# Performance work log

Measured on AMD Instinct MI355X. Metric: run time of the kernel, lower is better.

## Reference

```python
import jax, jax.numpy as jnp
import numpy as np

N_EMBD = 2048
HEAD_DIM = 128
N_CTX = 2048
BATCH = 8
SEQ = 2048


def setup_inputs() -> dict:
    key = jax.random.key(0)
    ks = jax.random.split(key, 7)
    s = 1.0 / np.sqrt(N_EMBD)
    x = jax.random.normal(ks[0], (BATCH, SEQ, N_EMBD), dtype=jnp.float32)
    # torch Linear params: weight (out, in), bias (out,)
    Wq = jax.random.uniform(ks[1], (HEAD_DIM, N_EMBD), jnp.float32, -s, s)
    bq = jax.random.uniform(ks[2], (HEAD_DIM,), jnp.float32, -s, s)
    Wk = jax.random.uniform(ks[3], (HEAD_DIM, N_EMBD), jnp.float32, -s, s)
    bk = jax.random.uniform(ks[4], (HEAD_DIM,), jnp.float32, -s, s)
    Wv = jax.random.uniform(ks[5], (HEAD_DIM, N_EMBD), jnp.float32, -s, s)
    bv = jax.random.uniform(ks[6], (HEAD_DIM,), jnp.float32, -s, s)
    return {"x": x, "Wq": Wq, "bq": bq, "Wk": Wk, "bk": bk, "Wv": Wv, "bv": bv}


def reference(x, Wq, bq, Wk, bk, Wv, bv):
    # projections: y = x @ W^T + b
    q = jnp.einsum('bse,de->bsd', x, Wq) + bq  # (B, S, D)
    k = jnp.einsum('bse,de->bsd', x, Wk) + bk
    v = jnp.einsum('bse,de->bsd', x, Wv) + bv
    seq = x.shape[1]
    scores = jnp.einsum('bqd,bkd->bqk', q, k)  # (B, S, S)
    # causal mask: strictly-upper-triangular positions set to -inf (before scaling, as in source)
    causal = jnp.triu(jnp.ones((seq, seq), dtype=bool), k=1)
    scores = jnp.where(causal[None, :, :], -jnp.inf, scores)
    # NOTE: source scales by sqrt(seq_size), not sqrt(head_dim)
    weight = jax.nn.softmax(scores / jnp.sqrt(jnp.float32(seq)), axis=-1)
    return jnp.einsum('bqk,bkd->bqd', weight, v)
```

## Files before the change

kernel.cpp:

```cpp
#include <hip/hip_runtime.h>
#include <cmath>

#define BATCH 8
#define SEQ   2048
#define NEMB  2048
#define HD    128
#define NROWS (BATCH * SEQ)

typedef __bf16 v8bf __attribute__((ext_vector_type(8)));
typedef float  f32x4 __attribute__((ext_vector_type(4)));

union U8 { v8bf v; __bf16 b[8]; unsigned short e[8]; };

__device__ inline void async16(void* lds, const void* g) {
  __builtin_amdgcn_global_load_lds(
      (const __attribute__((address_space(1))) unsigned int*)g,
      (__attribute__((address_space(3))) unsigned int*)lds, 16, 0, 0);
}

__device__ inline v8bf cvt8(float4 a, float4 b) {
  U8 u;
  u.b[0] = (__bf16)a.x; u.b[1] = (__bf16)a.y; u.b[2] = (__bf16)a.z; u.b[3] = (__bf16)a.w;
  u.b[4] = (__bf16)b.x; u.b[5] = (__bf16)b.y; u.b[6] = (__bf16)b.z; u.b[7] = (__bf16)b.w;
  return u.v;
}

__global__ __launch_bounds__(256) void wconv_kernel(
    const float* __restrict__ Wq, const float* __restrict__ Wk,
    const float* __restrict__ Wv, __bf16* __restrict__ out) {
  const int id = blockIdx.x;
  const int proj = id >> 6, blk = id & 63;
  const float* __restrict__ W = proj == 0 ? Wq : proj == 1 ? Wk : Wv;
  __bf16* __restrict__ o = out + (size_t)proj * (HD * NEMB);
  const int base = blk * 4096 + threadIdx.x * 16;
  const float4* s = (const float4*)(W + base);
  float4 f0 = s[0], f1 = s[1], f2 = s[2], f3 = s[3];
  *(v8bf*)(o + base) = cvt8(f0, f1);
  *(v8bf*)(o + base + 8) = cvt8(f2, f3);
}

__global__ __launch_bounds__(256, 3) void qkv_proj_kernel(
    const float* __restrict__ x, const __bf16* __restrict__ Wb,
    const float* __restrict__ bq, const float* __restrict__ bk,
    const float* __restrict__ bv,
    __bf16* __restrict__ Qb, __bf16* __restrict__ Kb, __bf16* __restrict__ Vb)
{
  const int bid0 = blockIdx.x;
  const int bid = ((bid0 & 7) * 96) + (bid0 >> 3);
  const int mt = bid / 3;
  const int proj = bid % 3;
  const __bf16* __restrict__ W = Wb + (size_t)proj * (HD * NEMB);
  const float* __restrict__ bias = proj == 0 ? bq : proj == 1 ? bk : bv;
  __bf16* __restrict__ Out = proj == 0 ? Qb : proj == 1 ? Kb : Vb;
  const int m0 = mt * 64;

  __shared__ __bf16 Asm[64 * 64];
  __shared__ __bf16 Bsm[128 * 64];

  const int t = threadIdx.x, lane = t & 63, w = t >> 6;
  const int wm = w >> 1, wn = w & 1;
  const int hi = lane >> 4, lo = lane & 15;

  const int arow = t >> 2, aq = t & 3;
  const float* axp = x + (size_t)(m0 + arow) * NEMB + aq * 16;
  char* aw0 = (char*)Asm + arow * 128 + (((aq * 2)     ^ (arow & 7)) << 4);
  char* aw1 = (char*)Asm + arow * 128 + (((aq * 2 + 1) ^ (arow & 7)) << 4);

  const __bf16* pb[4];
#pragma unroll
  for (int i = 0; i < 4; ++i) {
    const int r = (w * 4 + i) * 8 + (lane >> 3);
    const int c = (lane & 7) ^ (r & 7);
    pb[i] = W + (size_t)r * NEMB + c * 8;
  }

  f32x4 acc[2][4];
  const f32x4 fz = {0.f, 0.f, 0.f, 0.f};
#pragma unroll
  for (int m = 0; m < 2; ++m)
#pragma unroll
    for (int n = 0; n < 4; ++n) acc[m][n] = fz;

  float4 fa0, fa1, fa2, fa3;
  auto ALOAD = [&](int tt) {
    const float* p = axp + tt * 64;
    fa0 = *(const float4*)(p);
    fa1 = *(const float4*)(p + 4);
    fa2 = *(const float4*)(p + 8);
    fa3 = *(const float4*)(p + 12);
  };

  const int NT = NEMB / 64;
  ALOAD(0);
  for (int tt = 0; tt < NT; ++tt) {
    __syncthreads();
    {
      const int k0 = tt * 64;
#pragma unroll
      for (int i = 0; i < 4; ++i) async16((char*)Bsm + (w * 4 + i) * 1024, pb[i] + k0);
      *(v8bf*)aw0 = cvt8(fa0, fa1);
      *(v8bf*)aw1 = cvt8(fa2, fa3);
    }
    __syncthreads();
    if (tt + 1 < NT) ALOAD(tt + 1);

#pragma unroll
    for (int kk = 0; kk < 2; ++kk) {
      v8bf a[2], b[4];
      const int kc = kk * 4 + hi;
#pragma unroll
      for (int m = 0; m < 2; ++m) {
        const int r = wm * 32 + m * 16 + lo;
        a[m] = *(const v8bf*)((const char*)Asm + r * 128 + ((kc ^ (r & 7)) << 4));
      }
#pragma unroll
      for (int n = 0; n < 4; ++n) {
        const int r = wn * 64 + n * 16 + lo;
        b[n] = *(const v8bf*)((const char*)Bsm + r * 128 + ((kc ^ (r & 7)) << 4));
      }
#pragma unroll
      for (int m = 0; m < 2; ++m)
#pragma unroll
        for (int n = 0; n < 4; ++n)
          acc[m][n] = __builtin_amdgcn_mfma_f32_16x16x32_bf16(a[m], b[n], acc[m][n], 0, 0, 0);
    }
  }

#pragma unroll
  for (int n = 0; n < 4; ++n) {
    const int col = wn * 64 + n * 16 + lo;
    const float bi = bias[col];
#pragma unroll
    for (int m = 0; m < 2; ++m) {
#pragma unroll
      for (int r = 0; r < 4; ++r) {
        const int row = m0 + wm * 32 + m * 16 + hi * 4 + r;
        Out[(size_t)row * HD + col] = (__bf16)(acc[m][n][r] + bi);
      }
    }
  }
}

__global__ __launch_bounds__(256) void attn_kernel(
    const __bf16* __restrict__ Qb, const __bf16* __restrict__ Kb,
    const __bf16* __restrict__ Vb, float* __restrict__ Opart,
    float* __restrict__ Ml)
{
  const int bid0 = blockIdx.x;
  const int bid = ((bid0 & 7) << 6) + (bid0 >> 3);
  const int b = bid >> 6;
  const int qs = bid & 63;
  const int qt = qs >> 1;
  const int s  = qs & 1;
  const int q0 = qt * 64;
  const int half = (qt + 2) >> 1;
  const int kv_beg = s ? half : 0;
  const int kv_end = s ? (qt + 1) : half;
  const int nst = kv_end - kv_beg;

  const int t = threadIdx.x, lane = t & 63, w = t >> 6;
  const int hi = lane >> 4, lo = lane & 15;

  __shared__ __bf16 Ksm[2][64 * 128];
  __shared__ __bf16 Vtsm[2][128 * 64];
  __shared__ __bf16 Psm[4][16 * 64];

  v8bf aQ[4];
  {
    const __bf16* qp = Qb + ((size_t)(b * SEQ + q0 + w * 16 + lo)) * HD + hi * 8;
#pragma unroll
    for (int kk = 0; kk < 4; ++kk) aQ[kk] = *(const v8bf*)(qp + kk * 32);
  }

  const __bf16* kga[4];
#pragma unroll
  for (int i = 0; i < 4; ++i) {
    const int r = (w * 4 + i) * 4 + (lane >> 4);
    const int c = (lane & 15) ^ (r & 7);
    kga[i] = Kb + ((size_t)(b * SEQ) + r) * HD + c * 8;
  }

  const int keyg = t >> 4, dg = t & 15;
  U8 vv[4];

  f32x4 accO[8];
  const f32x4 fz = {0.f, 0.f, 0.f, 0.f};
#pragma unroll
  for (int n = 0; n < 8; ++n) accO[n] = fz;
  float m_s[4], l_s[4];
#pragma unroll
  for (int r = 0; r < 4; ++r) { m_s[r] = -INFINITY; l_s[r] = 0.f; }

  const float scale = 0.022097086912079608f;

  if (nst > 0) {
    auto STAGE_K = [&](int kv, int buf) {
      const size_t off = (size_t)kv * 64 * HD;
      char* kb = (char*)&Ksm[buf][0];
#pragma unroll
      for (int i = 0; i < 4; ++i) async16(kb + (w * 4 + i) * 1024, kga[i] + off);
    };
    auto LOAD_V = [&](int kv) {
      const __bf16* vp = Vb + ((size_t)(b * SEQ + kv * 64 + keyg * 4)) * HD + dg * 8;
#pragma unroll
      for (int j = 0; j < 4; ++j) vv[j].v = *(const v8bf*)(vp + (size_t)j * HD);
    };
    auto WRITE_VT = [&](int buf) {
      char* vb2 = (char*)&Vtsm[buf][0];
#pragma unroll
      for (int dd = 0; dd < 8; ++dd) {
        const int d = (dd + dg) & 7;
        ushort4 pk = make_ushort4(vv[0].e[d], vv[1].e[d], vv[2].e[d], vv[3].e[d]);
        const int row = dg * 8 + d;
        *(ushort4*)(vb2 + row * 128 + ((keyg * 8) ^ ((row & 7) << 4))) = pk;
      }
    };

    STAGE_K(kv_beg, 0);
    LOAD_V(kv_beg);
    WRITE_VT(0);
    __syncthreads();

    for (int t2 = 0; t2 < nst; ++t2) {
      const int kv = kv_beg + t2;
      const int cur = t2 & 1;
      const bool more = (t2 + 1 < nst);
      if (more) { STAGE_K(kv + 1, cur ^ 1); LOAD_V(kv + 1); }

      f32x4 accS[4];
#pragma unroll
      for (int n = 0; n < 4; ++n) accS[n] = fz;
      const char* ksm = (const char*)&Ksm[cur][0];
#pragma unroll
      for (int kk = 0; kk < 4; ++kk) {
        const int cb = kk * 64 + hi * 16;
        v8bf bk[4];
#pragma unroll
        for (int n = 0; n < 4; ++n) {
          const int r = n * 16 + lo;
          bk[n] = *(const v8bf*)(ksm + r * 256 + (cb ^ ((r & 7) << 4)));
        }
#pragma unroll
        for (int n = 0; n < 4; ++n)
          accS[n] = __builtin_amdgcn_mfma_f32_16x16x32_bf16(aQ[kk], bk[n], accS[n], 0, 0, 0);
      }

      float sv[4][4];
      const bool diag = (kv == qt);
#pragma unroll
      for (int n = 0; n < 4; ++n)
#pragma unroll
        for (int r = 0; r < 4; ++r) {
          float v = accS[n][r] * scale;
          if (diag) {
            const int key = kv * 64 + n * 16 + lo;
            const int qr = q0 + w * 16 + hi * 4 + r;
            if (key > qr) v = -INFINITY;
          }
          sv[n][r] = v;
        }

      float mx[4];
#pragma unroll
      for (int r = 0; r < 4; ++r) {
        mx[r] = fmaxf(fmaxf(sv[0][r], sv[1][r]), fmaxf(sv[2][r], sv[3][r]));
#pragma unroll
        for (int off = 1; off < 16; off <<= 1)
          mx[r] = fmaxf(mx[r], __shfl_xor(mx[r], off));
      }
      float corr[4], p[4][4], rs[4];
#pragma unroll
      for (int r = 0; r < 4; ++r) {
        const float mnew = fmaxf(m_s[r], mx[r]);
        corr[r] = __expf(m_s[r] - mnew);
        m_s[r] = mnew;
        rs[r] = 0.f;
      }
#pragma unroll
      for (int n = 0; n < 4; ++n)
#pragma unroll
        for (int r = 0; r < 4; ++r) {
          p[n][r] = __expf(sv[n][r] - m_s[r]);
          rs[r] += p[n][r];
        }
#pragma unroll
      for (int r = 0; r < 4; ++r) {
#pragma unroll
        for (int off = 1; off < 16; off <<= 1) rs[r] += __shfl_xor(rs[r], off);
        l_s[r] = l_s[r] * corr[r] + rs[r];
      }
#pragma unroll
      for (int n = 0; n < 8; ++n)
#pragma unroll
        for (int r = 0; r < 4; ++r) accO[n][r] *= corr[r];

#pragma unroll
      for (int n = 0; n < 4; ++n)
#pragma unroll
        for (int r = 0; r < 4; ++r) {
          const int row = hi * 4 + r;
          __bf16 h = (__bf16)p[n][r];
          *(unsigned short*)((char*)&Psm[w][0] + row * 128 +
                             (((n * 16 + lo) * 2) ^ ((row & 7) << 4))) =
              __builtin_bit_cast(unsigned short, h);
        }

      if (more) WRITE_VT(cur ^ 1);

      const char* vsm = (const char*)&Vtsm[cur][0];
#pragma unroll
      for (int k2 = 0; k2 < 2; ++k2) {
        const int cb = k2 * 64 + hi * 16;
        const v8bf aP = *(const v8bf*)((const char*)&Psm[w][0] + lo * 128 + (cb ^ ((lo & 7) << 4)));
#pragma unroll
        for (int n = 0; n < 8; ++n) {
          const int r = n * 16 + lo;
          const v8bf bv = *(const v8bf*)(vsm + r * 128 + (cb ^ ((r & 7) << 4)));
          accO[n] = __builtin_amdgcn_mfma_f32_16x16x32_bf16(aP, bv, accO[n], 0, 0, 0);
        }
      }
      if (more) __syncthreads();
    }
  }

#pragma unroll
  for (int r = 0; r < 4; ++r) {
    const int qr = q0 + w * 16 + hi * 4 + r;
    float* op = Opart + ((size_t)s * NROWS + b * SEQ + qr) * HD + lo;
#pragma unroll
    for (int n = 0; n < 8; ++n) op[n * 16] = accO[n][r];
    if (lo == 0) {
      float* mlp = Ml + ((size_t)s * NROWS + b * SEQ + qr) * 2;
      mlp[0] = m_s[r];
      mlp[1] = l_s[r];
    }
  }
}

__global__ __launch_bounds__(256) void combine_kernel(
    const float* __restrict__ Opart, const float* __restrict__ Ml,
    float* __restrict__ out)
{
  const int idx = blockIdx.x * 256 + threadIdx.x;
  const int row = idx >> 1, h = idx & 1;
  const float m0 = Ml[(size_t)row * 2],           l0 = Ml[(size_t)row * 2 + 1];
  const float m1 = Ml[((size_t)NROWS + row) * 2], l1 = Ml[((size_t)NROWS + row) * 2 + 1];
  const float M = fmaxf(m0, m1);
  const float e0 = __expf(m0 - M), e1 = __expf(m1 - M);
  const float inv = 1.f / (l0 * e0 + l1 * e1);
  const float4* p0 = (const float4*)(Opart + (size_t)row * HD + h * 64);
  const float4* p1 = (const float4*)(Opart + ((size_t)NROWS + row) * HD + h * 64);
  float4* po = (float4*)(out + (size_t)row * HD + h * 64);
#pragma unroll
  for (int j = 0; j < 16; ++j) {
    float4 a = p0[j], c = p1[j];
    float4 r;
    r.x = (a.x * e0 + c.x * e1) * inv;
    r.y = (a.y * e0 + c.y * e1) * inv;
    r.z = (a.z * e0 + c.z * e1) * inv;
    r.w = (a.w * e0 + c.w * e1) * inv;
    po[j] = r;
  }
}

extern "C" void kernel_launch(void* const* d_in, const int* in_sizes, int n_in,
                              void* d_out, int out_size, void* d_ws, size_t ws_size,
                              hipStream_t stream) {
  const float* x  = (const float*)d_in[0];
  const float* Wq = (const float*)d_in[1];
  const float* bq = (const float*)d_in[2];
  const float* Wk = (const float*)d_in[3];
  const float* bk = (const float*)d_in[4];
  const float* Wv = (const float*)d_in[5];
  const float* bv = (const float*)d_in[6];
  float* out = (float*)d_out;

  __bf16* Qb = (__bf16*)d_ws;
  __bf16* Kb = Qb + (size_t)NROWS * HD;
  __bf16* Vb = Kb + (size_t)NROWS * HD;
  __bf16* Wb = Vb + (size_t)NROWS * HD;
  float*  Opart = (float*)(Wb + (size_t)3 * HD * NEMB);
  float*  Ml    = Opart + (size_t)2 * NROWS * HD;

  wconv_kernel<<<dim3(3 * 64), dim3(256), 0, stream>>>(Wq, Wk, Wv, Wb);
  qkv_proj_kernel<<<dim3(256 * 3), dim3(256), 0, stream>>>(
      x, Wb, bq, bk, bv, Qb, Kb, Vb);
  attn_kernel<<<dim3(BATCH * 32 * 2), dim3(256), 0, stream>>>(Qb, Kb, Vb, Opart, Ml);
  combine_kernel<<<dim3(NROWS * 2 / 256), dim3(256), 0, stream>>>(Opart, Ml, out);
}
```

Before: 138.1 us.

## Replace LDS-staged QKV projection with direct-to-register double-buffered loads

The QKV projection kernel no longer stages x and W tiles through shared memory with barriers. Each wave loads its MFMA operand fragments straight from global memory into registers, double-buffered across k-tiles, and converts x to bf16 in registers. The tiling changes to 128 rows x 64 columns per block with no cross-wave sharing, so x and W are re-read more often from cache and global memory. Dropping the launch-bounds occupancy hint also raises register pressure.

Result: slower. 257.7 us (+86.6%).

```diff
diff --git a/kernel.cpp b/kernel.cpp
--- a/kernel.cpp
+++ b/kernel.cpp
@@ -11,6 +11,7 @@
 typedef float  f32x4 __attribute__((ext_vector_type(4)));
 
 union U8 { v8bf v; __bf16 b[8]; unsigned short e[8]; };
+union F4 { f32x4 v; float f[4]; };
 
 __device__ inline void async16(void* lds, const void* g) {
   __builtin_amdgcn_global_load_lds(
@@ -22,6 +23,13 @@
   U8 u;
   u.b[0] = (__bf16)a.x; u.b[1] = (__bf16)a.y; u.b[2] = (__bf16)a.z; u.b[3] = (__bf16)a.w;
   u.b[4] = (__bf16)b.x; u.b[5] = (__bf16)b.y; u.b[6] = (__bf16)b.z; u.b[7] = (__bf16)b.w;
+  return u.v;
+}
+
+__device__ inline v8bf cvt8v(f32x4 a, f32x4 b) {
+  U8 u;
+#pragma unroll
+  for (int q = 0; q < 4; ++q) { u.b[q] = (__bf16)a[q]; u.b[q + 4] = (__bf16)b[q]; }
   return u.v;
 }
 
@@ -39,7 +47,7 @@
   *(v8bf*)(o + base + 8) = cvt8(f2, f3);
 }
 
-__global__ __launch_bounds__(256, 3) void qkv_proj_kernel(
+__global__ __launch_bounds__(256) void qkv_proj_kernel(
     const float* __restrict__ x, const __bf16* __restrict__ Wb,
     const float* __restrict__ bq, const float* __restrict__ bk,
     const float* __restrict__ bv,
@@ -47,32 +55,26 @@
 {
   const int bid0 = blockIdx.x;
   const int bid = ((bid0 & 7) * 96) + (bid0 >> 3);
-  const int mt = bid / 3;
-  const int proj = bid % 3;
+  const int mt = bid / 6;
+  const int rem = bid % 6;
+  const int proj = rem >> 1;
+  const int nt = rem & 1;
   const __bf16* __restrict__ W = Wb + (size_t)proj * (HD * NEMB);
   const float* __restrict__ bias = proj == 0 ? bq : proj == 1 ? bk : bv;
   __bf16* __restrict__ Out = proj == 0 ? Qb : proj == 1 ? Kb : Vb;
-  const int m0 = mt * 64;
-
-  __shared__ __bf16 Asm[64 * 64];
-  __shared__ __bf16 Bsm[128 * 64];
 
   const int t = threadIdx.x, lane = t & 63, w = t >> 6;
-  const int wm = w >> 1, wn = w & 1;
   const int hi = lane >> 4, lo = lane & 15;
-
-  const int arow = t >> 2, aq = t & 3;
-  const float* axp = x + (size_t)(m0 + arow) * NEMB + aq * 16;
-  char* aw0 = (char*)Asm + arow * 128 + (((aq * 2)     ^ (arow & 7)) << 4);
-  char* aw1 = (char*)Asm + arow * 128 + (((aq * 2 + 1) ^ (arow & 7)) << 4);
-
-  const __bf16* pb[4];
-#pragma unroll
-  for (int i = 0; i < 4; ++i) {
-    const int r = (w * 4 + i) * 8 + (lane >> 3);
-    const int c = (lane & 7) ^ (r & 7);
-    pb[i] = W + (size_t)r * NEMB + c * 8;
-  }
+  const int row0 = mt * 128 + w * 32;
+  const int col0 = nt * 64;
+
+  const float* ax[2];
+  ax[0] = x + (size_t)(row0 + lo) * NEMB + hi * 8;
+  ax[1] = ax[0] + (size_t)16 * NEMB;
+  const __bf16* bw[4];
+#pragma unroll
+  for (int n = 0; n < 4; ++n)
+    bw[n] = W + (size_t)(col0 + n * 16 + lo) * NEMB + hi * 8;
 
   f32x4 acc[2][4];
   const f32x4 fz = {0.f, 0.f, 0.f, 0.f};
@@ -81,60 +83,59 @@
 #pragma unroll
     for (int n = 0; n < 4; ++n) acc[m][n] = fz;
 
-  float4 fa0, fa1, fa2, fa3;
-  auto ALOAD = [&](int tt) {
-    const float* p = axp + tt * 64;
-    fa0 = *(const float4*)(p);
-    fa1 = *(const float4*)(p + 4);
-    fa2 = *(const float4*)(p + 8);
-    fa3 = *(const float4*)(p + 12);
+  f32x4 A0[2][2][2], A1[2][2][2];
+  v8bf  B0[4][2],    B1[4][2];
+
+  auto LOADT = [&](f32x4 (&A)[2][2][2], v8bf (&B)[4][2], int tt) {
+    const int k0 = tt * 64;
+#pragma unroll
+    for (int m = 0; m < 2; ++m)
+#pragma unroll
+      for (int kk = 0; kk < 2; ++kk) {
+        const float* p = ax[m] + k0 + kk * 32;
+        A[m][kk][0] = *(const f32x4*)(p);
+        A[m][kk][1] = *(const f32x4*)(p + 4);
+      }
+#pragma unroll
+    for (int n = 0; n < 4; ++n)
+#pragma unroll
+      for (int kk = 0; kk < 2; ++kk)
+        B[n][kk] = *(const v8bf*)(bw[n] + k0 + kk * 32);
   };
+  auto STEP = [&](f32x4 (&A)[2][2][2], v8bf (&B)[4][2]) {
+    v8bf af[2][2];
+#pragma unroll
+    for (int m = 0; m < 2; ++m)
+#pragma unroll
+      for (int kk = 0; kk < 2; ++kk)
+        af[m][kk] = cvt8v(A[m][kk][0], A[m][kk][1]);
+#pragma unroll
+    for (int kk = 0; kk < 2; ++kk)
+#pragma unroll
+      for (int m = 0; m < 2; ++m)
+#pragma unroll
+        for (int n = 0; n < 4; ++n)
+          acc[m][n] = __builtin_amdgcn_mfma_f32_16x16x32_bf16(af[m][kk], B[n][kk], acc[m][n], 0, 0, 0);
+  };
 
   const int NT = NEMB / 64;
-  ALOAD(0);
-  for (int tt = 0; tt < NT; ++tt) {
-    __syncthreads();
-    {
-      const int k0 = tt * 64;
-#pragma unroll
-      for (int i = 0; i < 4; ++i) async16((char*)Bsm + (w * 4 + i) * 1024, pb[i] + k0);
-      *(v8bf*)aw0 = cvt8(fa0, fa1);
-      *(v8bf*)aw1 = cvt8(fa2, fa3);
-    }
-    __syncthreads();
-    if (tt + 1 < NT) ALOAD(tt + 1);
-
-#pragma unroll
-    for (int kk = 0; kk < 2; ++kk) {
-      v8bf a[2], b[4];
-      const int kc = kk * 4 + hi;
-#pragma unroll
-      for (int m = 0; m < 2; ++m) {
-        const int r = wm * 32 + m * 16 + lo;
-        a[m] = *(const v8bf*)((const char*)Asm + r * 128 + ((kc ^ (r & 7)) << 4));
-      }
-#pragma unroll
-      for (int n = 0; n < 4; ++n) {
-        const int r = wn * 64 + n * 16 + lo;
-        b[n] = *(const v8bf*)((const char*)Bsm + r * 128 + ((kc ^ (r & 7)) << 4));
-      }
-#pragma unroll
-      for (int m = 0; m < 2; ++m)
-#pragma unroll
-        for (int n = 0; n < 4; ++n)
-          acc[m][n] = __builtin_amdgcn_mfma_f32_16x16x32_bf16(a[m], b[n], acc[m][n], 0, 0, 0);
-    }
+  LOADT(A0, B0, 0);
+  for (int tt = 0; tt < NT; tt += 2) {
+    LOADT(A1, B1, tt + 1);
+    STEP(A0, B0);
+    if (tt + 2 < NT) LOADT(A0, B0, tt + 2);
+    STEP(A1, B1);
   }
 
 #pragma unroll
   for (int n = 0; n < 4; ++n) {
-    const int col = wn * 64 + n * 16 + lo;
+    const int col = col0 + n * 16 + lo;
     const float bi = bias[col];
 #pragma unroll
     for (int m = 0; m < 2; ++m) {
 #pragma unroll
       for (int r = 0; r < 4; ++r) {
-        const int row = m0 + wm * 32 + m * 16 + hi * 4 + r;
+        const int row = row0 + m * 16 + hi * 4 + r;
         Out[(size_t)row * HD + col] = (__bf16)(acc[m][n][r] + bi);
       }
     }
@@ -383,7 +384,7 @@
   float*  Ml    = Opart + (size_t)2 * NROWS * HD;
 
   wconv_kernel<<<dim3(3 * 64), dim3(256), 0, stream>>>(Wq, Wk, Wv, Wb);
-  qkv_proj_kernel<<<dim3(256 * 3), dim3(256), 0, stream>>>(
+  qkv_proj_kernel<<<dim3(128 * 3 * 2), dim3(256), 0, stream>>>(
       x, Wb, bq, bk, bv, Qb, Kb, Vb);
   attn_kernel<<<dim3(BATCH * 32 * 2), dim3(256), 0, stream>>>(Qb, Kb, Vb, Opart, Ml);
   combine_kernel<<<dim3(NROWS * 2 / 256), dim3(256), 0, stream>>>(Opart, Ml, out);
```

## Split attention KV range four ways, store bf16 partials, widen projection K-tile

Applied to the files above, without the earlier changes.

The attention kernel now splits each query tile's causal KV range into four chunks instead of two, doubling the grid so more blocks run in parallel and per-block work is more even. Partial outputs are stored as bf16 instead of fp32, and the combine kernel merges four partials per row. The QKV projection kernel doubles its K-tile to 128, halving the number of loop iterations and barriers at the cost of more LDS per block. Risks include bf16 rounding of the partial outputs, extra combine traffic, and lower occupancy in the projection kernel.

Measured after the change: 116.7 us. 15.5% less time.

```diff
diff --git a/kernel.cpp b/kernel.cpp
--- a/kernel.cpp
+++ b/kernel.cpp
@@ -54,24 +54,31 @@
   __bf16* __restrict__ Out = proj == 0 ? Qb : proj == 1 ? Kb : Vb;
   const int m0 = mt * 64;
 
-  __shared__ __bf16 Asm[64 * 64];
-  __shared__ __bf16 Bsm[128 * 64];
+  __shared__ __bf16 Asm[64 * 128];
+  __shared__ __bf16 Bsm[128 * 128];
 
   const int t = threadIdx.x, lane = t & 63, w = t >> 6;
   const int wm = w >> 1, wn = w & 1;
   const int hi = lane >> 4, lo = lane & 15;
 
-  const int arow = t >> 2, aq = t & 3;
-  const float* axp = x + (size_t)(m0 + arow) * NEMB + aq * 16;
-  char* aw0 = (char*)Asm + arow * 128 + (((aq * 2)     ^ (arow & 7)) << 4);
-  char* aw1 = (char*)Asm + arow * 128 + (((aq * 2 + 1) ^ (arow & 7)) << 4);
-
-  const __bf16* pb[4];
+  const float* pa[4];
+  int aw[4];
 #pragma unroll
   for (int i = 0; i < 4; ++i) {
-    const int r = (w * 4 + i) * 8 + (lane >> 3);
-    const int c = (lane & 7) ^ (r & 7);
+    const int r = (w * 4 + i) * 4 + (lane >> 4);
+    const int p = lane & 15;
+    pa[i] = x + (size_t)(m0 + r) * NEMB + p * 8;
+    aw[i] = r * 256 + ((p ^ (r & 7)) << 4);
+  }
+  const __bf16* pb[8];
+  char* lb[8];
+#pragma unroll
+  for (int i = 0; i < 8; ++i) {
+    const int j = w * 8 + i;
+    const int r = j * 4 + (lane >> 4);
+    const int c = (lane & 15) ^ (r & 7);
     pb[i] = W + (size_t)r * NEMB + c * 8;
+    lb[i] = (char*)Bsm + j * 1024;
   }
 
   f32x4 acc[2][4];
@@ -81,42 +88,47 @@
 #pragma unroll
     for (int n = 0; n < 4; ++n) acc[m][n] = fz;
 
-  float4 fa0, fa1, fa2, fa3;
+  float4 fa[4][2];
   auto ALOAD = [&](int tt) {
-    const float* p = axp + tt * 64;
-    fa0 = *(const float4*)(p);
-    fa1 = *(const float4*)(p + 4);
-    fa2 = *(const float4*)(p + 8);
-    fa3 = *(const float4*)(p + 12);
+#pragma unroll
+    for (int i = 0; i < 4; ++i) {
+      const float* p = pa[i] + tt * 128;
+      fa[i][0] = *(const float4*)(p);
+      fa[i][1] = *(const float4*)(p + 4);
+    }
   };
-
-  const int NT = NEMB / 64;
+  auto AWRITE = [&]() {
+#pragma unroll
+    for (int i = 0; i < 4; ++i)
+      *(v8bf*)((char*)Asm + aw[i]) = cvt8(fa[i][0], fa[i][1]);
+  };
+  auto STAGE_B = [&](int tt) {
+#pragma unroll
+    for (int i = 0; i < 8; ++i) async16(lb[i], pb[i] + tt * 128);
+  };
+
+  const int NT = NEMB / 128;
   ALOAD(0);
   for (int tt = 0; tt < NT; ++tt) {
     __syncthreads();
-    {
-      const int k0 = tt * 64;
-#pragma unroll
-      for (int i = 0; i < 4; ++i) async16((char*)Bsm + (w * 4 + i) * 1024, pb[i] + k0);
-      *(v8bf*)aw0 = cvt8(fa0, fa1);
-      *(v8bf*)aw1 = cvt8(fa2, fa3);
-    }
+    STAGE_B(tt);
+    AWRITE();
     __syncthreads();
     if (tt + 1 < NT) ALOAD(tt + 1);
 
 #pragma unroll
-    for (int kk = 0; kk < 2; ++kk) {
+    for (int kk = 0; kk < 4; ++kk) {
+      const int kc = kk * 4 + hi;
       v8bf a[2], b[4];
-      const int kc = kk * 4 + hi;
 #pragma unroll
       for (int m = 0; m < 2; ++m) {
         const int r = wm * 32 + m * 16 + lo;
-        a[m] = *(const v8bf*)((const char*)Asm + r * 128 + ((kc ^ (r & 7)) << 4));
+        a[m] = *(const v8bf*)((const char*)Asm + r * 256 + ((kc ^ (r & 7)) << 4));
       }
 #pragma unroll
       for (int n = 0; n < 4; ++n) {
         const int r = wn * 64 + n * 16 + lo;
-        b[n] = *(const v8bf*)((const char*)Bsm + r * 128 + ((kc ^ (r & 7)) << 4));
+        b[n] = *(const v8bf*)((const char*)Bsm + r * 256 + ((kc ^ (r & 7)) << 4));
       }
 #pragma unroll
       for (int m = 0; m < 2; ++m)
@@ -143,19 +155,18 @@
 
 __global__ __launch_bounds__(256) void attn_kernel(
     const __bf16* __restrict__ Qb, const __bf16* __restrict__ Kb,
-    const __bf16* __restrict__ Vb, float* __restrict__ Opart,
+    const __bf16* __restrict__ Vb, __bf16* __restrict__ Opart,
     float* __restrict__ Ml)
 {
   const int bid0 = blockIdx.x;
-  const int bid = ((bid0 & 7) << 6) + (bid0 >> 3);
-  const int b = bid >> 6;
-  const int qs = bid & 63;
-  const int qt = qs >> 1;
-  const int s  = qs & 1;
+  const int bid = ((bid0 & 7) << 7) + (bid0 >> 3);
+  const int b = bid >> 7;
+  const int q = bid & 127;
+  const int qt = q >> 2;
+  const int s  = q & 3;
   const int q0 = qt * 64;
-  const int half = (qt + 2) >> 1;
-  const int kv_beg = s ? half : 0;
-  const int kv_end = s ? (qt + 1) : half;
+  const int kv_beg = (s * (qt + 1)) >> 2;
+  const int kv_end = ((s + 1) * (qt + 1)) >> 2;
   const int nst = kv_end - kv_beg;
 
   const int t = threadIdx.x, lane = t & 63, w = t >> 6;
@@ -326,9 +337,9 @@
 #pragma unroll
   for (int r = 0; r < 4; ++r) {
     const int qr = q0 + w * 16 + hi * 4 + r;
-    float* op = Opart + ((size_t)s * NROWS + b * SEQ + qr) * HD + lo;
-#pragma unroll
-    for (int n = 0; n < 8; ++n) op[n * 16] = accO[n][r];
+    __bf16* op = Opart + ((size_t)s * NROWS + b * SEQ + qr) * HD + lo;
+#pragma unroll
+    for (int n = 0; n < 8; ++n) op[n * 16] = (__bf16)accO[n][r];
     if (lo == 0) {
       float* mlp = Ml + ((size_t)s * NROWS + b * SEQ + qr) * 2;
       mlp[0] = m_s[r];
@@ -338,28 +349,39 @@
 }
 
 __global__ __launch_bounds__(256) void combine_kernel(
-    const float* __restrict__ Opart, const float* __restrict__ Ml,
+    const __bf16* __restrict__ Opart, const float* __restrict__ Ml,
     float* __restrict__ out)
 {
   const int idx = blockIdx.x * 256 + threadIdx.x;
-  const int row = idx >> 1, h = idx & 1;
-  const float m0 = Ml[(size_t)row * 2],           l0 = Ml[(size_t)row * 2 + 1];
-  const float m1 = Ml[((size_t)NROWS + row) * 2], l1 = Ml[((size_t)NROWS + row) * 2 + 1];
-  const float M = fmaxf(m0, m1);
-  const float e0 = __expf(m0 - M), e1 = __expf(m1 - M);
-  const float inv = 1.f / (l0 * e0 + l1 * e1);
-  const float4* p0 = (const float4*)(Opart + (size_t)row * HD + h * 64);
-  const float4* p1 = (const float4*)(Opart + ((size_t)NROWS + row) * HD + h * 64);
-  float4* po = (float4*)(out + (size_t)row * HD + h * 64);
-#pragma unroll
-  for (int j = 0; j < 16; ++j) {
-    float4 a = p0[j], c = p1[j];
-    float4 r;
-    r.x = (a.x * e0 + c.x * e1) * inv;
-    r.y = (a.y * e0 + c.y * e1) * inv;
-    r.z = (a.z * e0 + c.z * e1) * inv;
-    r.w = (a.w * e0 + c.w * e1) * inv;
-    po[j] = r;
+  const int row = idx >> 2, ch = idx & 3;
+  float m[4], l[4];
+#pragma unroll
+  for (int s = 0; s < 4; ++s) {
+    const float* mlp = Ml + ((size_t)s * NROWS + row) * 2;
+    m[s] = mlp[0];
+    l[s] = mlp[1];
+  }
+  const float M = fmaxf(fmaxf(m[0], m[1]), fmaxf(m[2], m[3]));
+  float e[4], denom = 0.f;
+#pragma unroll
+  for (int s = 0; s < 4; ++s) { e[s] = __expf(m[s] - M); denom += l[s] * e[s]; }
+  const float inv = 1.f / denom;
+
+  float* po = out + (size_t)row * HD + ch * 32;
+#pragma unroll
+  for (int j = 0; j < 4; ++j) {
+    float sum[8];
+#pragma unroll
+    for (int q2 = 0; q2 < 8; ++q2) sum[q2] = 0.f;
+#pragma unroll
+    for (int s = 0; s < 4; ++s) {
+      U8 o;
+      o.v = *(const v8bf*)(Opart + ((size_t)s * NROWS + row) * HD + ch * 32 + j * 8);
+#pragma unroll
+      for (int q2 = 0; q2 < 8; ++q2) sum[q2] += (float)o.b[q2] * e[s];
+    }
+#pragma unroll
+    for (int q2 = 0; q2 < 8; ++q2) po[j * 8 + q2] = sum[q2] * inv;
   }
 }
 
@@ -379,12 +401,12 @@
   __bf16* Kb = Qb + (size_t)NROWS * HD;
   __bf16* Vb = Kb + (size_t)NROWS * HD;
   __bf16* Wb = Vb + (size_t)NROWS * HD;
-  float*  Opart = (float*)(Wb + (size_t)3 * HD * NEMB);
-  float*  Ml    = Opart + (size_t)2 * NROWS * HD;
+  __bf16* Opart = Wb + (size_t)3 * HD * NEMB;
+  float*  Ml = (float*)(Opart + (size_t)4 * NROWS * HD);
 
   wconv_kernel<<<dim3(3 * 64), dim3(256), 0, stream>>>(Wq, Wk, Wv, Wb);
   qkv_proj_kernel<<<dim3(256 * 3), dim3(256), 0, stream>>>(
       x, Wb, bq, bk, bv, Qb, Kb, Vb);
-  attn_kernel<<<dim3(BATCH * 32 * 2), dim3(256), 0, stream>>>(Qb, Kb, Vb, Opart, Ml);
-  combine_kernel<<<dim3(NROWS * 2 / 256), dim3(256), 0, stream>>>(Opart, Ml, out);
-}
+  attn_kernel<<<dim3(BATCH * 32 * 4), dim3(256), 0, stream>>>(Qb, Kb, Vb, Opart, Ml);
+  combine_kernel<<<dim3(NROWS * 4 / 256), dim3(256), 0, stream>>>(Opart, Ml, out);
+}
```
